# Performance work log

Hardware: AMD Instinct MI355X
Metric: run time of the kernel (lower is better)

The kernel has to match this reference:

```python
import jax, jax.numpy as jnp
import numpy as np
from jax import lax

B, T, IN_DIM, HIDDEN = 8, 4096, 1024, 1024


def setup_inputs() -> dict:
    key = jax.random.key(0)
    k_x, k_wd, k_wb = jax.random.split(key, 3)
    x = jax.random.normal(k_x, (B, T, IN_DIM), dtype=jnp.float32)
    h0 = jnp.zeros((B, HIDDEN), dtype=jnp.float32)
    # nn.Linear default init ~ U(-1/sqrt(in), 1/sqrt(in)); b_proj.weight ~ N(0, 0.02)
    lim = 1.0 / np.sqrt(IN_DIM)
    Wd = jax.random.uniform(k_wd, (HIDDEN, IN_DIM), jnp.float32, -lim, lim)
    bd = jnp.zeros((HIDDEN,), dtype=jnp.float32)
    Wb = 0.02 * jax.random.normal(k_wb, (HIDDEN, IN_DIM), dtype=jnp.float32)
    bb = jnp.zeros((HIDDEN,), dtype=jnp.float32)
    # 'hasani' init: A_log = log(linspace(0.5, 2.0, hidden))
    A_log = jnp.log(jnp.linspace(0.5, 2.0, HIDDEN, dtype=jnp.float32))
    return {"x": x, "h0": h0, "Wd": Wd, "bd": bd, "Wb": Wb, "bb": bb, "A_log": A_log}


def _combine(c1, c2):
    # composition of affine maps h -> a*h + b
    a1, b1 = c1
    a2, b2 = c2
    return a1 * a2, a2 * b1 + b2


def reference(x, h0, Wd, bd, Wb, bb, A_log):
    # projections: (B,T,in) @ (in,hidden)
    delta = jax.nn.softplus(jnp.einsum('bti,hi->bth', x, Wd) + bd)
    b_t = delta * (jnp.einsum('bti,hi->bth', x, Wb) + bb)
    A = jnp.exp(A_log)                      # (H,) decay rate
    A_t = jnp.exp(-delta * A)               # (B,T,H)
    # parallel (Blelloch/Heinsen-style) associative scan over T:
    # cumulative affine maps give h_t = A_cum_t * h0 + B_cum_t
    A_cum, B_cum = lax.associative_scan(_combine, (A_t, b_t), axis=1)
    h_full = A_cum * h0[:, None, :] + B_cum  # (B,T,H)
    return jnp.tanh(h_full)                  # bound=True
```

## Files before the change

### kernel.cpp

```cpp
#include <hip/hip_runtime.h>
#include <math.h>

#define B_DIM 8
#define T_DIM 4096
#define K_DIM 1024
#define H_DIM 1024
#define M_DIM (B_DIM * T_DIM)

#define CH 64
#define NC (T_DIM / CH)

typedef short bf16x8 __attribute__((ext_vector_type(8)));
typedef float f32x4  __attribute__((ext_vector_type(4)));

__device__ __forceinline__ unsigned short f2bf(float f) {
  unsigned int u = __builtin_bit_cast(unsigned int, f);
  u += 0x7FFFu + ((u >> 16) & 1u);
  return (unsigned short)(u >> 16);
}

__device__ __forceinline__ void gload_lds16(const void* g, void* l) {
  __builtin_amdgcn_global_load_lds(
      (const __attribute__((address_space(1))) unsigned int*)g,
      (__attribute__((address_space(3))) unsigned int*)l,
      16 , 0 , 0 );
}

__device__ __forceinline__ float softplus_fast(float x) {
  float e = __expf(-fabsf(x));
  return fmaxf(x, 0.f) + __logf(1.f + e);
}

__device__ __forceinline__ float tanh_fast(float x) {
  float e = __expf(2.f * x);
  return 1.f - 2.f * __builtin_amdgcn_rcpf(e + 1.f);
}

__global__ __launch_bounds__(256) void k_cvt(const float* __restrict__ in,
                                             unsigned short* __restrict__ out,
                                             int n8) {
  int i = blockIdx.x * 256 + threadIdx.x;
  if (i >= n8) return;
  float4 v0 = ((const float4*)in)[i * 2 + 0];
  float4 v1 = ((const float4*)in)[i * 2 + 1];
  bf16x8 r;
  r[0] = (short)f2bf(v0.x); r[1] = (short)f2bf(v0.y);
  r[2] = (short)f2bf(v0.z); r[3] = (short)f2bf(v0.w);
  r[4] = (short)f2bf(v1.x); r[5] = (short)f2bf(v1.y);
  r[6] = (short)f2bf(v1.z); r[7] = (short)f2bf(v1.w);
  ((bf16x8*)out)[i] = r;
}

__global__ __launch_bounds__(512, 4) void k_gemm_dual(
    const unsigned short* __restrict__ Xb,
    const unsigned short* __restrict__ Wdb,
    const unsigned short* __restrict__ Wbb,
    const float* __restrict__ bd,
    const float* __restrict__ bb,
    const float* __restrict__ A_log,
    float* __restrict__ a_out,
    float* __restrict__ b_out)
{
  __shared__ unsigned short As [128 * 32];
  __shared__ unsigned short Bs0[128 * 32];
  __shared__ unsigned short Bs1[128 * 32];

  const int tid  = threadIdx.x;
  const int bm   = blockIdx.x * 128;
  const int bn   = blockIdx.y * 128;
  const int w    = tid >> 6;
  const int lane = tid & 63;
  const int wm   = (w >> 2) * 64;
  const int wn   = (w & 3) * 32;

  f32x4 accd[4][2], accb[4][2];
  const f32x4 z4 = {0.f, 0.f, 0.f, 0.f};
  for (int m = 0; m < 4; m++)
    for (int n = 0; n < 2; n++) { accd[m][n] = z4; accb[m][n] = z4; }

  const int fr = lane & 15;
  const int kq = (lane >> 4) * 8;

  const int srow = tid >> 2;
  const int skk  = (tid & 3) * 8;

  for (int k0 = 0; k0 < K_DIM; k0 += 32) {
    size_t goffA = (size_t)(bm + srow) * K_DIM + (size_t)(k0 + skk);
    size_t goffB = (size_t)(bn + srow) * K_DIM + (size_t)(k0 + skk);
    gload_lds16(Xb  + goffA, &As [srow * 32 + skk]);
    gload_lds16(Wdb + goffB, &Bs0[srow * 32 + skk]);
    gload_lds16(Wbb + goffB, &Bs1[srow * 32 + skk]);
    __syncthreads();

    bf16x8 af[4], b0[2], b1[2];
#pragma unroll
    for (int m = 0; m < 4; m++)
      af[m] = *(const bf16x8*)&As[(wm + m * 16 + fr) * 32 + kq];
#pragma unroll
    for (int n = 0; n < 2; n++) {
      b0[n] = *(const bf16x8*)&Bs0[(wn + n * 16 + fr) * 32 + kq];
      b1[n] = *(const bf16x8*)&Bs1[(wn + n * 16 + fr) * 32 + kq];
    }
#pragma unroll
    for (int m = 0; m < 4; m++)
#pragma unroll
      for (int n = 0; n < 2; n++) {
        accd[m][n] = __builtin_amdgcn_mfma_f32_16x16x32_bf16(af[m], b0[n], accd[m][n], 0, 0, 0);
        accb[m][n] = __builtin_amdgcn_mfma_f32_16x16x32_bf16(af[m], b1[n], accb[m][n], 0, 0, 0);
      }
    __syncthreads();
  }

  const int col   = lane & 15;
  const int rbase = (lane >> 4) * 4;
#pragma unroll
  for (int n = 0; n < 2; n++) {
    int gn = bn + wn + n * 16 + col;
    float bdv = bd[gn];
    float bbv = bb[gn];
    float Ah  = __expf(A_log[gn]);
#pragma unroll
    for (int m = 0; m < 4; m++) {
#pragma unroll
      for (int r = 0; r < 4; r++) {
        int gm = bm + wm + m * 16 + rbase + r;
        float z1  = accd[m][n][r] + bdv;
        float z2  = accb[m][n][r] + bbv;
        float dlt = softplus_fast(z1);
        float av  = __expf(-dlt * Ah);
        size_t off = (size_t)gm * H_DIM + (size_t)gn;
        a_out[off] = av;
        b_out[off] = dlt * z2;
      }
    }
  }
}

__global__ __launch_bounds__(256) void k_scan_agg(
    const float* __restrict__ a_arr, const float* b_arr,
    float* __restrict__ aggA, float* __restrict__ aggB)
{
  int idx = blockIdx.x * 256 + threadIdx.x;
  int h   = idx & (H_DIM - 1);
  int bc  = idx >> 10;
  int c   = bc & (NC - 1);
  int b   = bc >> 6;
  size_t base = ((size_t)b * T_DIM + (size_t)c * CH) * H_DIM + (size_t)h;
  float A = 1.f, Bv = 0.f;
#pragma unroll 8
  for (int i = 0; i < CH; i++) {
    float at = a_arr[base + (size_t)i * H_DIM];
    float bt = b_arr[base + (size_t)i * H_DIM];
    Bv = fmaf(at, Bv, bt);
    A *= at;
  }
  aggA[idx] = A;
  aggB[idx] = Bv;
}

__global__ __launch_bounds__(256) void k_scan_chunks(
    const float* __restrict__ aggA, const float* __restrict__ aggB,
    const float* __restrict__ h0, float* __restrict__ hstart)
{
  int idx = blockIdx.x * 256 + threadIdx.x;
  int h   = idx & (H_DIM - 1);
  int b   = idx >> 10;
  float hc = h0[idx];
  for (int c = 0; c < NC; c++) {
    size_t o = ((size_t)(b * NC + c) << 10) + (size_t)h;
    hstart[o] = hc;
    hc = fmaf(aggA[o], hc, aggB[o]);
  }
}

__global__ __launch_bounds__(256) void k_scan_apply(
    const float* __restrict__ a_arr, const float* b_arr,
    const float* __restrict__ hstart, float* out)
{
  int idx = blockIdx.x * 256 + threadIdx.x;
  int h   = idx & (H_DIM - 1);
  int bc  = idx >> 10;
  int c   = bc & (NC - 1);
  int b   = bc >> 6;
  size_t base = ((size_t)b * T_DIM + (size_t)c * CH) * H_DIM + (size_t)h;
  float hc = hstart[idx];
#pragma unroll 4
  for (int i = 0; i < CH; i++) {
    size_t o = base + (size_t)i * H_DIM;
    float at = a_arr[o];
    float bt = b_arr[o];
    hc = fmaf(at, hc, bt);
    out[o] = tanh_fast(hc);
  }
}

extern "C" void kernel_launch(void* const* d_in, const int* in_sizes, int n_in,
                              void* d_out, int out_size, void* d_ws, size_t ws_size,
                              hipStream_t stream) {
  const float* x     = (const float*)d_in[0];
  const float* h0    = (const float*)d_in[1];
  const float* Wd    = (const float*)d_in[2];
  const float* bd    = (const float*)d_in[3];
  const float* Wb    = (const float*)d_in[4];
  const float* bb    = (const float*)d_in[5];
  const float* A_log = (const float*)d_in[6];
  float* out = (float*)d_out;

  char* ws = (char*)d_ws;
  unsigned short* xb   = (unsigned short*)(ws + 0);
  unsigned short* wdb  = (unsigned short*)(ws + 67108864);
  unsigned short* wbb  = (unsigned short*)(ws + 69206016);
  float*          aarr = (float*)(ws + 71303168);
  float*          aggA = (float*)(ws + 205520896);
  float*          aggB = (float*)(ws + 207618048);
  float*          hst  = (float*)(ws + 209715200);
  float*          barr = out;

  k_cvt<<<(M_DIM * K_DIM / 8) / 256, 256, 0, stream>>>(x, xb, M_DIM * K_DIM / 8);
  k_cvt<<<(H_DIM * K_DIM / 8) / 256, 256, 0, stream>>>(Wd, wdb, H_DIM * K_DIM / 8);
  k_cvt<<<(H_DIM * K_DIM / 8) / 256, 256, 0, stream>>>(Wb, wbb, H_DIM * K_DIM / 8);

  dim3 gg(M_DIM / 128, H_DIM / 128);
  k_gemm_dual<<<gg, 512, 0, stream>>>(xb, wdb, wbb, bd, bb, A_log, aarr, barr);

  k_scan_agg   <<<(B_DIM * NC * H_DIM) / 256, 256, 0, stream>>>(aarr, barr, aggA, aggB);
  k_scan_chunks<<<(B_DIM * H_DIM) / 256,      256, 0, stream>>>(aggA, aggB, h0, hst);
  k_scan_apply <<<(B_DIM * NC * H_DIM) / 256, 256, 0, stream>>>(aarr, barr, hst, out);
}
```

Baseline: 364.3 us.

## Fuse chunk aggregate scan into GEMM epilogue and widen K tile with swizzled LDS

The per-chunk affine aggregates are now computed inside the GEMM epilogue: each lane combines its four rows, then lanes exchange segment aggregates via shuffles to form the 64-step chunk aggregate. This removes the separate k_scan_agg kernel, which re-read the full a and b arrays from memory. The GEMM K tile also doubles to 64 with an XOR-swizzled LDS layout to reduce bank conflicts and halve the number of barriers. LDS use per block doubles, which may reduce occupancy.

```diff
diff --git a/kernel.cpp b/kernel.cpp
--- a/kernel.cpp
+++ b/kernel.cpp
@@ -9,6 +9,7 @@
 
 #define CH 64
 #define NC (T_DIM / CH)
+#define BK 64
 
 typedef short bf16x8 __attribute__((ext_vector_type(8)));
 typedef float f32x4  __attribute__((ext_vector_type(4)));
@@ -59,11 +60,13 @@
     const float* __restrict__ bb,
     const float* __restrict__ A_log,
     float* __restrict__ a_out,
-    float* __restrict__ b_out)
+    float* __restrict__ b_out,
+    float* __restrict__ aggA,
+    float* __restrict__ aggB)
 {
-  __shared__ unsigned short As [128 * 32];
-  __shared__ unsigned short Bs0[128 * 32];
-  __shared__ unsigned short Bs1[128 * 32];
+  __shared__ unsigned short As [128 * BK];
+  __shared__ unsigned short Bs0[128 * BK];
+  __shared__ unsigned short Bs1[128 * BK];
 
   const int tid  = threadIdx.x;
   const int bm   = blockIdx.x * 128;
@@ -79,48 +82,64 @@
     for (int n = 0; n < 2; n++) { accd[m][n] = z4; accb[m][n] = z4; }
 
   const int fr = lane & 15;
-  const int kq = (lane >> 4) * 8;
-
-  const int srow = tid >> 2;
-  const int skk  = (tid & 3) * 8;
-
-  for (int k0 = 0; k0 < K_DIM; k0 += 32) {
-    size_t goffA = (size_t)(bm + srow) * K_DIM + (size_t)(k0 + skk);
-    size_t goffB = (size_t)(bn + srow) * K_DIM + (size_t)(k0 + skk);
-    gload_lds16(Xb  + goffA, &As [srow * 32 + skk]);
-    gload_lds16(Wdb + goffB, &Bs0[srow * 32 + skk]);
-    gload_lds16(Wbb + goffB, &Bs1[srow * 32 + skk]);
+  const int hi = lane >> 4;
+
+  for (int k0 = 0; k0 < K_DIM; k0 += BK) {
+#pragma unroll
+    for (int i = 0; i < 2; i++) {
+      int idx = i * 512 + tid;
+      int row = idx >> 3;
+      int cg  = (idx & 7) ^ (row & 7);
+      size_t goffA = (size_t)(bm + row) * K_DIM + (size_t)(k0 + cg * 8);
+      size_t goffB = (size_t)(bn + row) * K_DIM + (size_t)(k0 + cg * 8);
+      gload_lds16(Xb  + goffA, (char*)As  + idx * 16);
+      gload_lds16(Wdb + goffB, (char*)Bs0 + idx * 16);
+      gload_lds16(Wbb + goffB, (char*)Bs1 + idx * 16);
+    }
     __syncthreads();
 
-    bf16x8 af[4], b0[2], b1[2];
-#pragma unroll
-    for (int m = 0; m < 4; m++)
-      af[m] = *(const bf16x8*)&As[(wm + m * 16 + fr) * 32 + kq];
-#pragma unroll
-    for (int n = 0; n < 2; n++) {
-      b0[n] = *(const bf16x8*)&Bs0[(wn + n * 16 + fr) * 32 + kq];
-      b1[n] = *(const bf16x8*)&Bs1[(wn + n * 16 + fr) * 32 + kq];
-    }
-#pragma unroll
-    for (int m = 0; m < 4; m++)
+#pragma unroll
+    for (int ks = 0; ks < 2; ks++) {
+      bf16x8 af[4], b0[2], b1[2];
+#pragma unroll
+      for (int m = 0; m < 4; m++) {
+        int row = wm + m * 16 + fr;
+        int ch  = (ks * 4 + hi) ^ (row & 7);
+        af[m] = *(const bf16x8*)&As[row * BK + ch * 8];
+      }
 #pragma unroll
       for (int n = 0; n < 2; n++) {
-        accd[m][n] = __builtin_amdgcn_mfma_f32_16x16x32_bf16(af[m], b0[n], accd[m][n], 0, 0, 0);
-        accb[m][n] = __builtin_amdgcn_mfma_f32_16x16x32_bf16(af[m], b1[n], accb[m][n], 0, 0, 0);
-      }
+        int row = wn + n * 16 + fr;
+        int ch  = (ks * 4 + hi) ^ (row & 7);
+        b0[n] = *(const bf16x8*)&Bs0[row * BK + ch * 8];
+        b1[n] = *(const bf16x8*)&Bs1[row * BK + ch * 8];
+      }
+#pragma unroll
+      for (int m = 0; m < 4; m++)
+#pragma unroll
+        for (int n = 0; n < 2; n++) {
+          accd[m][n] = __builtin_amdgcn_mfma_f32_16x16x32_bf16(af[m], b0[n], accd[m][n], 0, 0, 0);
+          accb[m][n] = __builtin_amdgcn_mfma_f32_16x16x32_bf16(af[m], b1[n], accb[m][n], 0, 0, 0);
+        }
+    }
     __syncthreads();
   }
 
-  const int col   = lane & 15;
-  const int rbase = (lane >> 4) * 4;
+  const int col    = lane & 15;
+  const int rbase  = hi * 4;
+  const int bidx   = bm >> 12;
+  const int cchunk = ((bm & (T_DIM - 1)) + wm) >> 6;
+
 #pragma unroll
   for (int n = 0; n < 2; n++) {
     int gn = bn + wn + n * 16 + col;
     float bdv = bd[gn];
     float bbv = bb[gn];
     float Ah  = __expf(A_log[gn]);
+    float segA[4], segB[4];
 #pragma unroll
     for (int m = 0; m < 4; m++) {
+      float sA = 1.f, sB = 0.f;
 #pragma unroll
       for (int r = 0; r < 4; r++) {
         int gm = bm + wm + m * 16 + rbase + r;
@@ -128,34 +147,32 @@
         float z2  = accb[m][n][r] + bbv;
         float dlt = softplus_fast(z1);
         float av  = __expf(-dlt * Ah);
+        float bv  = dlt * z2;
         size_t off = (size_t)gm * H_DIM + (size_t)gn;
         a_out[off] = av;
-        b_out[off] = dlt * z2;
-      }
-    }
-  }
-}
-
-__global__ __launch_bounds__(256) void k_scan_agg(
-    const float* __restrict__ a_arr, const float* b_arr,
-    float* __restrict__ aggA, float* __restrict__ aggB)
-{
-  int idx = blockIdx.x * 256 + threadIdx.x;
-  int h   = idx & (H_DIM - 1);
-  int bc  = idx >> 10;
-  int c   = bc & (NC - 1);
-  int b   = bc >> 6;
-  size_t base = ((size_t)b * T_DIM + (size_t)c * CH) * H_DIM + (size_t)h;
-  float A = 1.f, Bv = 0.f;
-#pragma unroll 8
-  for (int i = 0; i < CH; i++) {
-    float at = a_arr[base + (size_t)i * H_DIM];
-    float bt = b_arr[base + (size_t)i * H_DIM];
-    Bv = fmaf(at, Bv, bt);
-    A *= at;
-  }
-  aggA[idx] = A;
-  aggB[idx] = Bv;
+        b_out[off] = bv;
+        sB = fmaf(av, sB, bv);
+        sA *= av;
+      }
+      segA[m] = sA; segB[m] = sB;
+    }
+    float chA = 1.f, chB = 0.f;
+#pragma unroll
+    for (int m = 0; m < 4; m++) {
+#pragma unroll
+      for (int h2 = 0; h2 < 4; h2++) {
+        float sa = __shfl(segA[m], col + h2 * 16, 64);
+        float sb = __shfl(segB[m], col + h2 * 16, 64);
+        chB = fmaf(sa, chB, sb);
+        chA *= sa;
+      }
+    }
+    if (lane < 16) {
+      size_t o = ((size_t)(bidx * NC + cchunk) << 10) + (size_t)gn;
+      aggA[o] = chA;
+      aggB[o] = chB;
+    }
+  }
 }
 
 __global__ __launch_bounds__(256) void k_scan_chunks(
@@ -221,9 +238,9 @@
   k_cvt<<<(H_DIM * K_DIM / 8) / 256, 256, 0, stream>>>(Wb, wbb, H_DIM * K_DIM / 8);
 
   dim3 gg(M_DIM / 128, H_DIM / 128);
-  k_gemm_dual<<<gg, 512, 0, stream>>>(xb, wdb, wbb, bd, bb, A_log, aarr, barr);
-
-  k_scan_agg   <<<(B_DIM * NC * H_DIM) / 256, 256, 0, stream>>>(aarr, barr, aggA, aggB);
+  k_gemm_dual<<<gg, 512, 0, stream>>>(xb, wdb, wbb, bd, bb, A_log,
+                                      aarr, barr, aggA, aggB);
+
   k_scan_chunks<<<(B_DIM * H_DIM) / 256,      256, 0, stream>>>(aggA, aggB, h0, hst);
   k_scan_apply <<<(B_DIM * NC * H_DIM) / 256, 256, 0, stream>>>(aarr, barr, hst, out);
 }
```

After: 337.0 us. 1.08x faster.

## Fuse dual GEMM and chunked scan into one persistent kernel per batch/column strip

Applied to the files above, without the earlier changes.

Replaces the separate dual GEMM and the three scan kernels with one kernel. Each of 256 workgroups owns one batch and a 32-column strip and walks sequentially over T in 256-row tiles. The scan is done in registers, through wave shuffles and a small LDS carry, so the 128MB intermediate a/b arrays are never written to or read back from HBM. The GEMM gains a double-buffered LDS pipeline with XOR swizzle and BK=64. In exchange, the GEMM now runs serially per strip with only 256 workgroups and recomputes the X tile for each column strip, so X is read from global memory 32 times instead of 8.

```diff
diff --git a/kernel.cpp b/kernel.cpp
--- a/kernel.cpp
+++ b/kernel.cpp
@@ -6,9 +6,8 @@
 #define K_DIM 1024
 #define H_DIM 1024
 #define M_DIM (B_DIM * T_DIM)
-
-#define CH 64
-#define NC (T_DIM / CH)
+#define BK 64
+#define NTT 256
 
 typedef short bf16x8 __attribute__((ext_vector_type(8)));
 typedef float f32x4  __attribute__((ext_vector_type(4)));
@@ -51,147 +50,178 @@
   ((bf16x8*)out)[i] = r;
 }
 
-__global__ __launch_bounds__(512, 4) void k_gemm_dual(
+__global__ __launch_bounds__(512, 2) void k_mega(
     const unsigned short* __restrict__ Xb,
     const unsigned short* __restrict__ Wdb,
     const unsigned short* __restrict__ Wbb,
     const float* __restrict__ bd,
     const float* __restrict__ bb,
     const float* __restrict__ A_log,
-    float* __restrict__ a_out,
-    float* __restrict__ b_out)
+    const float* __restrict__ h0,
+    float* __restrict__ out)
 {
-  __shared__ unsigned short As [128 * 32];
-  __shared__ unsigned short Bs0[128 * 32];
-  __shared__ unsigned short Bs1[128 * 32];
-
-  const int tid  = threadIdx.x;
-  const int bm   = blockIdx.x * 128;
-  const int bn   = blockIdx.y * 128;
+  __shared__ unsigned short As[2][256 * BK];
+  __shared__ unsigned short Bs[2][64 * BK];
+  __shared__ float totA[4][32], totB[4][32];
+  __shared__ float h_state[32];
+
+  const int tid   = threadIdx.x;
+  const int wg    = blockIdx.x;
+  const int batch = wg & 7;
+  const int jn    = wg >> 3;
+  const int bn    = jn * 32;
+
   const int w    = tid >> 6;
   const int lane = tid & 63;
-  const int wm   = (w >> 2) * 64;
-  const int wn   = (w & 3) * 32;
-
-  f32x4 accd[4][2], accb[4][2];
+  const int c    = w >> 1;
+  const int g    = w & 1;
+  const int fr   = lane & 15;
+  const int hi   = lane >> 4;
+  const int lcol = g * 16 + fr;
+  const int gcol = bn + lcol;
+
+  const float bdv = bd[gcol];
+  const float bbv = bb[gcol];
+  const float Ah  = __expf(A_log[gcol]);
+
+  const unsigned short* gA[4];
+  int ldsA[4];
+#pragma unroll
+  for (int jj = 0; jj < 4; jj++) {
+    int idx = jj * 512 + tid;
+    int row = idx >> 3;
+    int cg  = (idx & 7) ^ (row & 7);
+    ldsA[jj] = idx * 16;
+    gA[jj] = Xb + (((size_t)(batch * T_DIM + row)) << 10) + (size_t)(cg * 8);
+  }
+  const unsigned short* gB;
+  int ldsB;
+  {
+    int idx = tid;
+    int vr  = idx >> 3;
+    int cg  = (idx & 7) ^ (vr & 7);
+    ldsB = idx * 16;
+    int h = bn + (vr >> 5) * 16 + (vr & 15);
+    const unsigned short* Wsrc = (vr & 16) ? Wbb : Wdb;
+    gB = Wsrc + (((size_t)h) << 10) + (size_t)(cg * 8);
+  }
+
+  const int ch0 = hi ^ (fr & 7);
+  const char* bA0 = (const char*)As + ((c * 64 + fr) * 128 + ch0 * 16);
+  const char* bA1 = (const char*)As + ((c * 64 + fr) * 128 + (ch0 ^ 4) * 16);
+  const char* bB0 = (const char*)Bs + ((g * 32 + fr) * 128 + ch0 * 16);
+  const char* bB1 = (const char*)Bs + ((g * 32 + fr) * 128 + (ch0 ^ 4) * 16);
+
+#define STAGE(TT, D)                                                          \
+  do {                                                                        \
+    int aOff = (((TT) >> 4) << 18) + (((TT) & 15) << 6);                      \
+    int bOff = ((TT) & 15) << 6;                                              \
+    _Pragma("unroll")                                                         \
+    for (int jj = 0; jj < 4; jj++)                                            \
+      gload_lds16(gA[jj] + aOff, (char*)As[D] + ldsA[jj]);                    \
+    gload_lds16(gB + bOff, (char*)Bs[D] + ldsB);                              \
+  } while (0)
+
+#define TILE(TT, D)                                                           \
+  do {                                                                        \
+    if ((TT) < NTT - 1) STAGE((TT) + 1, (D) ^ 1);                             \
+    bf16x8 Af[8], Bf[4];                                                      \
+    _Pragma("unroll")                                                         \
+    for (int mm = 0; mm < 4; mm++) {                                          \
+      Af[mm * 2 + 0] = *(const bf16x8*)(bA0 + (D) * 32768 + mm * 2048);       \
+      Af[mm * 2 + 1] = *(const bf16x8*)(bA1 + (D) * 32768 + mm * 2048);       \
+    }                                                                         \
+    _Pragma("unroll")                                                         \
+    for (int nn = 0; nn < 2; nn++) {                                          \
+      Bf[nn * 2 + 0] = *(const bf16x8*)(bB0 + (D) * 8192 + nn * 2048);        \
+      Bf[nn * 2 + 1] = *(const bf16x8*)(bB1 + (D) * 8192 + nn * 2048);        \
+    }                                                                         \
+    __builtin_amdgcn_s_setprio(1);                                            \
+    _Pragma("unroll")                                                         \
+    for (int mm = 0; mm < 4; mm++)                                            \
+      _Pragma("unroll")                                                       \
+      for (int nn = 0; nn < 2; nn++)                                          \
+        _Pragma("unroll")                                                     \
+        for (int kk = 0; kk < 2; kk++)                                        \
+          acc[mm][nn] = __builtin_amdgcn_mfma_f32_16x16x32_bf16(              \
+              Af[mm * 2 + kk], Bf[nn * 2 + kk], acc[mm][nn], 0, 0, 0);        \
+    __builtin_amdgcn_s_setprio(0);                                            \
+    asm volatile("s_waitcnt vmcnt(0)" ::: "memory");                          \
+    __builtin_amdgcn_s_barrier();                                             \
+  } while (0)
+
+  STAGE(0, 0);
+  if (tid < 32) h_state[tid] = h0[(batch << 10) + bn + tid];
+  asm volatile("s_waitcnt vmcnt(0)" ::: "memory");
+  __syncthreads();
+
   const f32x4 z4 = {0.f, 0.f, 0.f, 0.f};
-  for (int m = 0; m < 4; m++)
-    for (int n = 0; n < 2; n++) { accd[m][n] = z4; accb[m][n] = z4; }
-
-  const int fr = lane & 15;
-  const int kq = (lane >> 4) * 8;
-
-  const int srow = tid >> 2;
-  const int skk  = (tid & 3) * 8;
-
-  for (int k0 = 0; k0 < K_DIM; k0 += 32) {
-    size_t goffA = (size_t)(bm + srow) * K_DIM + (size_t)(k0 + skk);
-    size_t goffB = (size_t)(bn + srow) * K_DIM + (size_t)(k0 + skk);
-    gload_lds16(Xb  + goffA, &As [srow * 32 + skk]);
-    gload_lds16(Wdb + goffB, &Bs0[srow * 32 + skk]);
-    gload_lds16(Wbb + goffB, &Bs1[srow * 32 + skk]);
-    __syncthreads();
-
-    bf16x8 af[4], b0[2], b1[2];
-#pragma unroll
-    for (int m = 0; m < 4; m++)
-      af[m] = *(const bf16x8*)&As[(wm + m * 16 + fr) * 32 + kq];
-#pragma unroll
-    for (int n = 0; n < 2; n++) {
-      b0[n] = *(const bf16x8*)&Bs0[(wn + n * 16 + fr) * 32 + kq];
-      b1[n] = *(const bf16x8*)&Bs1[(wn + n * 16 + fr) * 32 + kq];
-    }
-#pragma unroll
-    for (int m = 0; m < 4; m++)
-#pragma unroll
-      for (int n = 0; n < 2; n++) {
-        accd[m][n] = __builtin_amdgcn_mfma_f32_16x16x32_bf16(af[m], b0[n], accd[m][n], 0, 0, 0);
-        accb[m][n] = __builtin_amdgcn_mfma_f32_16x16x32_bf16(af[m], b1[n], accb[m][n], 0, 0, 0);
-      }
-    __syncthreads();
-  }
-
-  const int col   = lane & 15;
-  const int rbase = (lane >> 4) * 4;
-#pragma unroll
-  for (int n = 0; n < 2; n++) {
-    int gn = bn + wn + n * 16 + col;
-    float bdv = bd[gn];
-    float bbv = bb[gn];
-    float Ah  = __expf(A_log[gn]);
+
+#pragma unroll 1
+  for (int mt = 0; mt < 16; mt++) {
+    f32x4 acc[4][2];
+#pragma unroll
+    for (int m = 0; m < 4; m++) { acc[m][0] = z4; acc[m][1] = z4; }
+
+#pragma unroll 1
+    for (int kp = 0; kp < 8; kp++) {
+      int tt = mt * 16 + kp * 2;
+      TILE(tt, 0);
+      TILE(tt + 1, 1);
+    }
+
+    float rA[4], rB[4], wAp[4][4], wBp[4][4];
 #pragma unroll
     for (int m = 0; m < 4; m++) {
+      float A_ = 1.f, B_ = 0.f;
 #pragma unroll
       for (int r = 0; r < 4; r++) {
-        int gm = bm + wm + m * 16 + rbase + r;
-        float z1  = accd[m][n][r] + bdv;
-        float z2  = accb[m][n][r] + bbv;
+        float z1  = acc[m][0][r] + bdv;
+        float z2  = acc[m][1][r] + bbv;
         float dlt = softplus_fast(z1);
         float av  = __expf(-dlt * Ah);
-        size_t off = (size_t)gm * H_DIM + (size_t)gn;
-        a_out[off] = av;
-        b_out[off] = dlt * z2;
+        float bv  = dlt * z2;
+        B_ = fmaf(av, B_, bv);
+        A_ *= av;
+        wAp[m][r] = A_; wBp[m][r] = B_;
       }
+      rA[m] = A_; rB[m] = B_;
+    }
+    float cA = 1.f, cB = 0.f, eA[4], eB[4];
+#pragma unroll
+    for (int rho = 0; rho < 16; rho++) {
+      if ((rho & 3) == hi) { eA[rho >> 2] = cA; eB[rho >> 2] = cB; }
+      float sa = __shfl(rA[rho >> 2], (rho & 3) * 16 + fr, 64);
+      float sb = __shfl(rB[rho >> 2], (rho & 3) * 16 + fr, 64);
+      cB = fmaf(sa, cB, sb);
+      cA *= sa;
+    }
+    if (hi == 0) { totA[c][lcol] = cA; totB[c][lcol] = cB; }
+    __syncthreads();
+    float hs = h_state[lcol];
+#pragma unroll
+    for (int cc = 0; cc < 3; cc++) {
+      float t2 = fmaf(totA[cc][lcol], hs, totB[cc][lcol]);
+      hs = (cc < c) ? t2 : hs;
+    }
+    __syncthreads();
+    if (c == 3 && hi == 0) h_state[lcol] = fmaf(cA, hs, cB);
+
+    size_t obase = (((size_t)(batch * T_DIM + mt * 256 + c * 64 + hi * 4)) << 10)
+                   + (size_t)gcol;
+#pragma unroll
+    for (int m = 0; m < 4; m++) {
+#pragma unroll
+      for (int r = 0; r < 4; r++) {
+        float aT = eA[m] * wAp[m][r];
+        float bT = fmaf(wAp[m][r], eB[m], wBp[m][r]);
+        float h  = fmaf(aT, hs, bT);
+        out[obase + ((size_t)(m * 16 + r) << 10)] = tanh_fast(h);
+      }
     }
   }
-}
-
-__global__ __launch_bounds__(256) void k_scan_agg(
-    const float* __restrict__ a_arr, const float* b_arr,
-    float* __restrict__ aggA, float* __restrict__ aggB)
-{
-  int idx = blockIdx.x * 256 + threadIdx.x;
-  int h   = idx & (H_DIM - 1);
-  int bc  = idx >> 10;
-  int c   = bc & (NC - 1);
-  int b   = bc >> 6;
-  size_t base = ((size_t)b * T_DIM + (size_t)c * CH) * H_DIM + (size_t)h;
-  float A = 1.f, Bv = 0.f;
-#pragma unroll 8
-  for (int i = 0; i < CH; i++) {
-    float at = a_arr[base + (size_t)i * H_DIM];
-    float bt = b_arr[base + (size_t)i * H_DIM];
-    Bv = fmaf(at, Bv, bt);
-    A *= at;
-  }
-  aggA[idx] = A;
-  aggB[idx] = Bv;
-}
-
-__global__ __launch_bounds__(256) void k_scan_chunks(
-    const float* __restrict__ aggA, const float* __restrict__ aggB,
-    const float* __restrict__ h0, float* __restrict__ hstart)
-{
-  int idx = blockIdx.x * 256 + threadIdx.x;
-  int h   = idx & (H_DIM - 1);
-  int b   = idx >> 10;
-  float hc = h0[idx];
-  for (int c = 0; c < NC; c++) {
-    size_t o = ((size_t)(b * NC + c) << 10) + (size_t)h;
-    hstart[o] = hc;
-    hc = fmaf(aggA[o], hc, aggB[o]);
-  }
-}
-
-__global__ __launch_bounds__(256) void k_scan_apply(
-    const float* __restrict__ a_arr, const float* b_arr,
-    const float* __restrict__ hstart, float* out)
-{
-  int idx = blockIdx.x * 256 + threadIdx.x;
-  int h   = idx & (H_DIM - 1);
-  int bc  = idx >> 10;
-  int c   = bc & (NC - 1);
-  int b   = bc >> 6;
-  size_t base = ((size_t)b * T_DIM + (size_t)c * CH) * H_DIM + (size_t)h;
-  float hc = hstart[idx];
-#pragma unroll 4
-  for (int i = 0; i < CH; i++) {
-    size_t o = base + (size_t)i * H_DIM;
-    float at = a_arr[o];
-    float bt = b_arr[o];
-    hc = fmaf(at, hc, bt);
-    out[o] = tanh_fast(hc);
-  }
+#undef TILE
+#undef STAGE
 }
 
 extern "C" void kernel_launch(void* const* d_in, const int* in_sizes, int n_in,
@@ -207,23 +237,13 @@
   float* out = (float*)d_out;
 
   char* ws = (char*)d_ws;
-  unsigned short* xb   = (unsigned short*)(ws + 0);
-  unsigned short* wdb  = (unsigned short*)(ws + 67108864);
-  unsigned short* wbb  = (unsigned short*)(ws + 69206016);
-  float*          aarr = (float*)(ws + 71303168);
-  float*          aggA = (float*)(ws + 205520896);
-  float*          aggB = (float*)(ws + 207618048);
-  float*          hst  = (float*)(ws + 209715200);
-  float*          barr = out;
+  unsigned short* xb  = (unsigned short*)(ws + 0);
+  unsigned short* wdb = (unsigned short*)(ws + 67108864);
+  unsigned short* wbb = (unsigned short*)(ws + 69206016);
 
   k_cvt<<<(M_DIM * K_DIM / 8) / 256, 256, 0, stream>>>(x, xb, M_DIM * K_DIM / 8);
   k_cvt<<<(H_DIM * K_DIM / 8) / 256, 256, 0, stream>>>(Wd, wdb, H_DIM * K_DIM / 8);
   k_cvt<<<(H_DIM * K_DIM / 8) / 256, 256, 0, stream>>>(Wb, wbb, H_DIM * K_DIM / 8);
 
-  dim3 gg(M_DIM / 128, H_DIM / 128);
-  k_gemm_dual<<<gg, 512, 0, stream>>>(xb, wdb, wbb, bd, bb, A_log, aarr, barr);
-
-  k_scan_agg   <<<(B_DIM * NC * H_DIM) / 256, 256, 0, stream>>>(aarr, barr, aggA, aggB);
-  k_scan_chunks<<<(B_DIM * H_DIM) / 256,      256, 0, stream>>>(aggA, aggB, h0, hst);
-  k_scan_apply <<<(B_DIM * NC * H_DIM) / 256, 256, 0, stream>>>(aarr, barr, hst, out);
-}
+  k_mega<<<256, 512, 0, stream>>>(xb, wdb, wbb, bd, bb, A_log, h0, out);
+}
```

After: 316.4 us. -13.1%, faster.
